# Kernel tuning notes

Hardware: AMD Instinct MI355X
Metric: run time of the kernel (lower is better)

The kernel has to match this reference:

```python
import jax, jax.numpy as jnp
import numpy as np

B, L, D_MODEL = 8, 256, 256
D_STATE, D_INNER, DT_RANK, D_CONV = 16, 512, 16, 4


def _ln(x, g, b, eps):
    mu = x.mean(-1, keepdims=True)
    var = ((x - mu) ** 2).mean(-1, keepdims=True)
    return (x - mu) * jax.lax.rsqrt(var + eps) * g + b


def _ssm(x, W_in, conv_w, conv_b, W_x, W_dt, b_dt, A_log, Dp, W_out):
    # x: (B, L, D_MODEL) -- standard Mamba selective-scan block
    xz = x @ W_in                                  # (B,L,2*Di)
    xc, z = jnp.split(xz, 2, axis=-1)
    K = conv_w.shape[-1]
    xp = jnp.pad(xc, ((0, 0), (K - 1, 0), (0, 0)))  # causal depthwise conv
    xc = sum(xp[:, k:k + L, :] * conv_w[:, k] for k in range(K)) + conv_b
    xc = jax.nn.silu(xc)
    x_dbl = xc @ W_x                               # (B,L,R+2S)
    dt, Bm, Cm = jnp.split(x_dbl, [DT_RANK, DT_RANK + D_STATE], axis=-1)
    dt = jax.nn.softplus(dt @ W_dt + b_dt)         # (B,L,Di)
    A = -jnp.exp(A_log)                            # (Di,S)
    dA = jnp.exp(dt[..., None] * A)                # (B,L,Di,S)
    dBx = dt[..., None] * Bm[:, :, None, :] * xc[..., None]

    def step(h, inp):
        dA_t, dBx_t, C_t = inp
        h = dA_t * h + dBx_t                       # (B,Di,S)
        y = jnp.einsum('bds,bs->bd', h, C_t)
        return h, y

    h0 = jnp.zeros((xc.shape[0], D_INNER, D_STATE), xc.dtype)
    xs = (dA.transpose(1, 0, 2, 3), dBx.transpose(1, 0, 2, 3), Cm.transpose(1, 0, 2))
    _, ys = jax.lax.scan(step, h0, xs)             # (L,B,Di)
    y = ys.transpose(1, 0, 2) + xc * Dp
    y = y * jax.nn.silu(z)
    return y @ W_out


def _basic(x, ln_g, ln_b, ssm_params):
    # Basic_Block: ReLU(SSM(LN(x))) + x  (drop_path=0, attn_drop=0)
    return jax.nn.relu(_ssm(_ln(x, ln_g, ln_b, 1e-6), *ssm_params)) + x


def setup_inputs() -> dict:
    key = jax.random.key(0)
    ks = jax.random.split(key, 32)

    def n(k, shape, s=0.02):
        return jax.random.normal(k, shape, dtype=jnp.float32) * s

    inp = {}
    inp['x_spa'] = jax.random.normal(ks[0], (B, L, D_MODEL), dtype=jnp.float32)
    inp['x_spe'] = jax.random.normal(ks[1], (B, L, D_MODEL), dtype=jnp.float32)
    i = 2
    A_init = jnp.log(jnp.tile(jnp.arange(1, D_STATE + 1, dtype=jnp.float32), (D_INNER, 1)))
    for p in ('spa', 'spe'):
        inp[p + '_ln_g'] = jnp.ones((D_MODEL,), jnp.float32)
        inp[p + '_ln_b'] = jnp.zeros((D_MODEL,), jnp.float32)
        inp[p + '_W_in'] = n(ks[i], (D_MODEL, 2 * D_INNER)); i += 1
        inp[p + '_conv_w'] = n(ks[i], (D_INNER, D_CONV), 0.1); i += 1
        inp[p + '_conv_b'] = jnp.zeros((D_INNER,), jnp.float32)
        inp[p + '_W_x'] = n(ks[i], (D_INNER, DT_RANK + 2 * D_STATE)); i += 1
        inp[p + '_W_dt'] = n(ks[i], (DT_RANK, D_INNER), 0.1); i += 1
        inp[p + '_b_dt'] = n(ks[i], (D_INNER,), 0.1); i += 1
        inp[p + '_A_log'] = A_init
        inp[p + '_D'] = jnp.ones((D_INNER,), jnp.float32)
        inp[p + '_W_out'] = n(ks[i], (D_INNER, D_MODEL)); i += 1
    inp['sc_W'] = n(ks[i], (D_MODEL, D_MODEL)); i += 1
    inp['sc_b'] = jnp.zeros((D_MODEL,), jnp.float32)
    inp['sc_ln_g'] = jnp.ones((D_MODEL,), jnp.float32)
    inp['sc_ln_b'] = jnp.zeros((D_MODEL,), jnp.float32)
    inp['fusion_W'] = n(ks[i], (D_MODEL, D_MODEL))
    return inp


def reference(x_spa, x_spe,
              spa_ln_g, spa_ln_b, spa_W_in, spa_conv_w, spa_conv_b, spa_W_x,
              spa_W_dt, spa_b_dt, spa_A_log, spa_D, spa_W_out,
              spe_ln_g, spe_ln_b, spe_W_in, spe_conv_w, spe_conv_b, spe_W_x,
              spe_W_dt, spe_b_dt, spe_A_log, spe_D, spe_W_out,
              sc_W, sc_b, sc_ln_g, sc_ln_b, fusion_W):
    # shared shortcut: Linear + LayerNorm (eps=1e-5)
    ident_spa = _ln(x_spa @ sc_W + sc_b, sc_ln_g, sc_ln_b, 1e-5)
    ident_spe = _ln(x_spe @ sc_W + sc_b, sc_ln_g, sc_ln_b, 1e-5)
    spa_p = (spa_W_in, spa_conv_w, spa_conv_b, spa_W_x, spa_W_dt, spa_b_dt, spa_A_log, spa_D, spa_W_out)
    spe_p = (spe_W_in, spe_conv_w, spe_conv_b, spe_W_x, spe_W_dt, spe_b_dt, spe_A_log, spe_D, spe_W_out)
    a = _basic(x_spa, spa_ln_g, spa_ln_b, spa_p)
    e = _basic(x_spe, spe_ln_g, spe_ln_b, spe_p)
    # fusion gate: mean-pool both branches, Linear(no bias) + sigmoid, broadcast-mul
    fw = jax.nn.sigmoid(((a.mean(1) + e.mean(1)) * 0.5) @ fusion_W)[:, None, :]
    a = a * fw
    e = e * fw
    return (a + ident_spa, e + ident_spe)
```

## Files before the change

kernel.cpp:

```cpp
#include <hip/hip_runtime.h>
#include <hip/hip_bf16.h>
#include <math.h>

#define BD 8
#define LD 256
#define DM 256
#define DS 16
#define DI 512
#define RK 16

#define NROWS (2*BD*LD)
#define HALF_ROWS (BD*LD)

typedef __attribute__((ext_vector_type(8))) short bhalf8;
typedef __attribute__((ext_vector_type(4))) float f32x4;

__device__ __forceinline__ float siluf(float x){ return x / (1.f + __expf(-x)); }
__device__ __forceinline__ float softplusf(float x){
  return fmaxf(x, 0.f) + log1pf(__expf(-fabsf(x)));
}
__device__ __forceinline__ unsigned short f2bf(float f){
  __hip_bfloat16 h = __float2bfloat16(f);
  return *reinterpret_cast<unsigned short*>(&h);
}


__global__ __launch_bounds__(256) void k_prep(
    const float* __restrict__ Wi_spa, const float* __restrict__ Wi_spe,
    const float* __restrict__ Wo_spa, const float* __restrict__ Wo_spe,
    const float* __restrict__ scW,
    const float* __restrict__ Wx_spa, const float* __restrict__ Wx_spe,
    const float* __restrict__ x_spa, const float* __restrict__ x_spe,
    const float* __restrict__ g_spa, const float* __restrict__ b_spa,
    const float* __restrict__ g_spe, const float* __restrict__ b_spe,
    unsigned short* __restrict__ Wt_i_spa, unsigned short* __restrict__ Wt_i_spe,
    unsigned short* __restrict__ Wt_o_spa, unsigned short* __restrict__ Wt_o_spe,
    unsigned short* __restrict__ scWt,
    unsigned short* __restrict__ Wxt_spa, unsigned short* __restrict__ Wxt_spe,
    unsigned short* __restrict__ xnbf, unsigned short* __restrict__ xbf,
    float* __restrict__ pooled)
{
  __shared__ __align__(16) unsigned char smem[59904];
  int b = blockIdx.x;
  int tid = threadIdx.x;
  if (b == 60){
    for (int i=tid; i<BD*DM; i+=256) pooled[i] = 0.f;
    return;
  }
  if (b >= 61){
    float (*xst)[260] = (float (*)[260])smem;
    float (*red)[16]  = (float (*)[16])(smem + 16640);
    float *mu = (float*)(smem + 17664);
    float *rs = (float*)(smem + 17728);
    int r0g = (b - 61) * 16;
    int branch = r0g >= HALF_ROWS;
    const float* xb = branch ? x_spe : x_spa;
    const float* g  = branch ? g_spe : g_spa;
    const float* be = branch ? b_spe : b_spa;
    int rr0 = branch ? r0g - HALF_ROWS : r0g;
    for (int p=0;p<4;p++){
      int i4 = tid + 256*p;
      int r = i4 >> 6, c4 = (i4 & 63)*4;
      *(float4*)&xst[r][c4] = *(const float4*)(xb + (rr0+r)*DM + c4);
    }
    __syncthreads();
    {
      int row = tid >> 4, seg = tid & 15;
      float s = 0.f, s2 = 0.f;
      #pragma unroll
      for (int i=0;i<4;i++){
        float4 v = *(float4*)&xst[row][seg*16 + i*4];
        s  += v.x+v.y+v.z+v.w;
        s2 += v.x*v.x + v.y*v.y + v.z*v.z + v.w*v.w;
      }
      red[row][seg] = s;
      __syncthreads();
      if (seg == 0){
        float t=0.f;
        #pragma unroll
        for (int i=0;i<16;i++) t += red[row][i];
        mu[row] = t * (1.f/DM);
      }
      __syncthreads();
      red[row][seg] = s2;
      __syncthreads();
      if (seg == 0){
        float t=0.f;
        #pragma unroll
        for (int i=0;i<16;i++) t += red[row][i];
        float m = mu[row];
        rs[row] = rsqrtf(t*(1.f/DM) - m*m + 1e-6f);
      }
    }
    __syncthreads();
    for (int p=0;p<4;p++){
      int i4 = tid + 256*p;
      int r = i4 >> 6, c4 = (i4 & 63)*4;
      float4 v  = *(float4*)&xst[r][c4];
      float4 gv = *(const float4*)(g + c4);
      float4 bv = *(const float4*)(be + c4);
      float m = mu[r], rv = rs[r];
      unsigned int rlo = (unsigned int)f2bf(v.x) | ((unsigned int)f2bf(v.y) << 16);
      unsigned int rhi = (unsigned int)f2bf(v.z) | ((unsigned int)f2bf(v.w) << 16);
      *(uint2*)&xbf[(r0g+r)*DM + c4] = make_uint2(rlo, rhi);
      unsigned int nlo = (unsigned int)f2bf((v.x-m)*rv*gv.x + bv.x)
                       | ((unsigned int)f2bf((v.y-m)*rv*gv.y + bv.y) << 16);
      unsigned int nhi = (unsigned int)f2bf((v.z-m)*rv*gv.z + bv.z)
                       | ((unsigned int)f2bf((v.w-m)*rv*gv.w + bv.w) << 16);
      *(uint2*)&xnbf[(r0g+r)*DM + c4] = make_uint2(nlo, nhi);
    }
    return;
  }
  if (b >= 52){
    int bb = b - 52;
    int branch = bb >> 2, chunk = bb & 3;
    int k0 = chunk*128;
    const float* Wx = branch ? Wx_spe : Wx_spa;
    unsigned short* Wxt = branch ? Wxt_spe : Wxt_spa;
    float (*tile2)[49] = (float (*)[49])(smem + 34816);
    for (int i=tid; i<128*48; i+=256){
      int kk = i/48, c = i - kk*48;
      tile2[kk][c] = Wx[(k0+kk)*48 + c];
    }
    __syncthreads();
    for (int i=tid; i<64*128; i+=256){
      int cc = i >> 7, kk = i & 127;
      float v = (cc < 48) ? tile2[kk][cc] : 0.f;
      int kg = k0 + kk;
      int ct = cc >> 4, m16 = cc & 15;
      int ks = kg >> 5, quad = (kg >> 3) & 3, j = kg & 7;
      Wxt[((ct*16 + ks)*64 + quad*16 + m16)*8 + j] = f2bf(v);
    }
    return;
  }
  unsigned short (*tile)[68] = (unsigned short (*)[68])smem;
  const float* W; unsigned short* Wt; int N, K, c0, k0;
  if (b < 32){
    int bb = b & 15;
    W  = (b < 16) ? Wi_spa  : Wi_spe;
    Wt = (b < 16) ? Wt_i_spa: Wt_i_spe;
    N = 1024; K = 256; c0 = (bb >> 2)*256; k0 = (bb & 3)*64;
  } else if (b < 48){
    int bb = b - 32; int h = bb >> 3; bb &= 7;
    W  = h ? Wo_spe  : Wo_spa;
    Wt = h ? Wt_o_spe: Wt_o_spa;
    N = 256; K = 512; c0 = 0; k0 = bb*64;
  } else {
    int bb = b - 48;
    W = scW; Wt = scWt;
    N = 256; K = 256; c0 = 0; k0 = bb*64;
  }
  int c = c0 + tid;
  #pragma unroll 8
  for (int kk=0; kk<64; kk++)
    tile[tid][kk] = f2bf(W[(k0+kk)*N + c]);
  __syncthreads();
  int ksegs = K >> 5;
  for (int p=0; p<16; p++){
    int i = tid + 256*p;
    int cl = i >> 4, kq = (i & 15)*4;
    int cg = c0 + cl;
    int ct = cg >> 4, m16 = cg & 15;
    int kg = k0 + kq;
    int ks = kg >> 5, quad = (kg >> 3) & 3, j = kg & 7;
    uint2 v = *(const uint2*)&tile[cl][kq];
    *(uint2*)&Wt[((ct*ksegs + ks)*64 + quad*16 + m16)*8 + j] = v;
  }
}

__global__ __launch_bounds__(256) void k_gemm1(
    const unsigned short* __restrict__ xnbf, const unsigned short* __restrict__ xbf,
    const unsigned short* __restrict__ Wt_spa, const unsigned short* __restrict__ Wt_spe,
    const unsigned short* __restrict__ scWt, const float* __restrict__ sc_b,
    const float* __restrict__ ln_g, const float* __restrict__ ln_b,
    float* __restrict__ xc_raw, float* __restrict__ szout, float* __restrict__ ident)
{
  __shared__ unsigned short At[16][264];
  __shared__ float Dt[16][260];
  __shared__ float red[16][16];
  __shared__ float mu[16], rs[16];
  int tid = threadIdx.x;
  int bi = blockIdx.x;
  int w = tid >> 6, lane = tid & 63;
  int m16 = lane & 15, quad = lane >> 4;
  if (bi < 1024){
    int rg = bi >> 2, cg = bi & 3;
    int r0 = rg * 16;
    int branch = (r0 >= HALF_ROWS);
    const unsigned short* Wt = branch ? Wt_spe : Wt_spa;
    for (int p=0;p<2;p++){
      int i = tid + 256*p;
      int r = i >> 5, oct = (i & 31)*8;
      *(uint4*)&At[r][oct] = *(const uint4*)&xnbf[(r0+r)*DM + oct];
    }
    __syncthreads();
    bhalf8 af[8];
    #pragma unroll
    for (int ks=0; ks<8; ks++)
      af[ks] = *(const bhalf8*)&At[m16][ks*32 + quad*8];
    f32x4 acc[4];
    #pragma unroll
    for (int ct=0; ct<4; ct++) acc[ct] = (f32x4)(0.f);
    #pragma unroll
    for (int ks=0; ks<8; ks++){
      #pragma unroll
      for (int ct=0; ct<4; ct++){
        int f = (cg*16 + w*4 + ct)*8 + ks;
        bhalf8 bf = *(const bhalf8*)&Wt[f*512 + lane*8];
        acc[ct] = __builtin_amdgcn_mfma_f32_16x16x32_bf16(af[ks], bf, acc[ct], 0,0,0);
      }
    }
    bool isz = (cg >= 2);
    float* outp = isz ? szout : xc_raw;
    int cbase = (cg & 1)*256 + w*64;
    #pragma unroll
    for (int ct=0; ct<4; ct++){
      #pragma unroll
      for (int e=0;e<4;e++){
        int row = r0 + quad*4 + e;
        int col = cbase + ct*16 + m16;
        float v = acc[ct][e];
        if (isz) v = siluf(v);
        outp[row*DI + col] = v;
      }
    }
  } else {
    int r0 = (bi - 1024) * 16;
    for (int p=0;p<2;p++){
      int i = tid + 256*p;
      int r = i >> 5, oct = (i & 31)*8;
      *(uint4*)&At[r][oct] = *(const uint4*)&xbf[(r0+r)*DM + oct];
    }
    __syncthreads();
    bhalf8 af[8];
    #pragma unroll
    for (int ks=0; ks<8; ks++)
      af[ks] = *(const bhalf8*)&At[m16][ks*32 + quad*8];
    f32x4 acc[4];
    #pragma unroll
    for (int ct=0; ct<4; ct++) acc[ct] = (f32x4)(0.f);
    #pragma unroll
    for (int ks=0; ks<8; ks++){
      #pragma unroll
      for (int ct=0; ct<4; ct++){
        int f = (w*4 + ct)*8 + ks;
        bhalf8 bf = *(const bhalf8*)&scWt[f*512 + lane*8];
        acc[ct] = __builtin_amdgcn_mfma_f32_16x16x32_bf16(af[ks], bf, acc[ct], 0,0,0);
      }
    }
    #pragma unroll
    for (int ct=0; ct<4; ct++){
      #pragma unroll
      for (int e=0;e<4;e++){
        int row = quad*4 + e;
        int col = w*64 + ct*16 + m16;
        Dt[row][col] = acc[ct][e] + sc_b[col];
      }
    }
    __syncthreads();
    {
      int row = tid >> 4, seg = tid & 15;
      float s = 0.f, s2 = 0.f;
      #pragma unroll
      for (int i=0;i<4;i++){
        float4 v = *(const float4*)&Dt[row][seg*16 + i*4];
        s  += v.x+v.y+v.z+v.w;
        s2 += v.x*v.x + v.y*v.y + v.z*v.z + v.w*v.w;
      }
      red[row][seg] = s;
      __syncthreads();
      if (seg == 0){
        float t=0.f;
        #pragma unroll
        for (int i=0;i<16;i++) t += red[row][i];
        mu[row] = t * (1.f/DM);
      }
      __syncthreads();
      red[row][seg] = s2;
      __syncthreads();
      if (seg == 0){
        float t=0.f;
        #pragma unroll
        for (int i=0;i<16;i++) t += red[row][i];
        float m = mu[row];
        rs[row] = rsqrtf(t*(1.f/DM) - m*m + 1e-5f);
      }
    }
    __syncthreads();
    float gg = ln_g[tid], bb = ln_b[tid];
    #pragma unroll
    for (int r=0;r<16;r++)
      ident[(r0+r)*DM + tid] = (Dt[r][tid]-mu[r])*rs[r]*gg + bb;
  }
}

__global__ __launch_bounds__(256) void k_convdbl(
    const float* __restrict__ cw_spa, const float* __restrict__ cb_spa,
    const float* __restrict__ cw_spe, const float* __restrict__ cb_spe,
    const float* __restrict__ xc_raw,
    const unsigned short* __restrict__ Wxt_spa, const unsigned short* __restrict__ Wxt_spe,
    const float* __restrict__ Wdt_spa, const float* __restrict__ bdt_spa,
    const float* __restrict__ Wdt_spe, const float* __restrict__ bdt_spe,
    float* __restrict__ xc, float* __restrict__ dt,
    float* __restrict__ Bm, float* __restrict__ Cm)
{
  __shared__ unsigned short At[16][520];
  __shared__ float xdbl[16][18];
  int tid = threadIdx.x;
  int r0 = blockIdx.x * 16;
  int branch = r0 >= HALF_ROWS;
  int l0 = r0 & (LD-1);
  const float* cw = branch ? cw_spe : cw_spa;
  const float* cb = branch ? cb_spe : cb_spa;
  const unsigned short* Wxt = branch ? Wxt_spe : Wxt_spa;
  const float* Wdt = branch ? Wdt_spe : Wdt_spa;
  const float* bdt = branch ? bdt_spe : bdt_spa;
  {
    int c = tid*2;
    float4 w0 = *(const float4*)(cw + 4*c);
    float4 w1 = *(const float4*)(cw + 4*(c+1));
    float2 bias = *(const float2*)(cb + c);
    float2 h0, h1, h2;
    if (l0 > 0){
      h0 = *(const float2*)(xc_raw + (r0-3)*DI + c);
      h1 = *(const float2*)(xc_raw + (r0-2)*DI + c);
      h2 = *(const float2*)(xc_raw + (r0-1)*DI + c);
    } else {
      h0 = make_float2(0.f,0.f); h1 = h0; h2 = h0;
    }
    #pragma unroll
    for (int r=0;r<16;r++){
      float2 cur = *(const float2*)(xc_raw + (r0+r)*DI + c);
      float vx = bias.x;
      vx = fmaf(h0.x, w0.x, vx); vx = fmaf(h1.x, w0.y, vx);
      vx = fmaf(h2.x, w0.z, vx); vx = fmaf(cur.x, w0.w, vx);
      float vy = bias.y;
      vy = fmaf(h0.y, w1.x, vy); vy = fmaf(h1.y, w1.y, vy);
      vy = fmaf(h2.y, w1.z, vy); vy = fmaf(cur.y, w1.w, vy);
      vx = siluf(vx); vy = siluf(vy);
      *(float2*)(xc + (r0+r)*DI + c) = make_float2(vx, vy);
      unsigned int pk = (unsigned int)f2bf(vx) | ((unsigned int)f2bf(vy) << 16);
      *(unsigned int*)&At[r][c] = pk;
      h0 = h1; h1 = h2; h2 = cur;
    }
  }
  __syncthreads();
  int w = tid >> 6, lane = tid & 63;
  int m16 = lane & 15, quad = lane >> 4;
  f32x4 acc = (f32x4)(0.f);
  #pragma unroll
  for (int ks=0; ks<16; ks++){
    bhalf8 a = *(const bhalf8*)&At[m16][ks*32 + quad*8];
    int f = w*16 + ks;
    bhalf8 bf = *(const bhalf8*)&Wxt[f*512 + lane*8];
    acc = __builtin_amdgcn_mfma_f32_16x16x32_bf16(a, bf, acc, 0,0,0);
  }
  #pragma unroll
  for (int e=0;e<4;e++){
    int row = quad*4 + e;
    float v = acc[e];
    if (w == 0)      xdbl[row][m16] = v;
    else if (w == 1) Bm[(r0+row)*DS + m16] = v;
    else if (w == 2) Cm[(r0+row)*DS + m16] = v;
  }
  __syncthreads();
  float wdt0[16], wdt1[16];
  #pragma unroll
  for (int j=0;j<16;j++){ wdt0[j]=Wdt[j*DI+tid]; wdt1[j]=Wdt[j*DI+tid+256]; }
  float b0 = bdt[tid], b1 = bdt[tid+256];
  #pragma unroll
  for (int r=0;r<16;r++){
    float a0=b0, a1=b1;
    #pragma unroll
    for (int j=0;j<16;j++){
      float xv = xdbl[r][j];
      a0 = fmaf(xv, wdt0[j], a0);
      a1 = fmaf(xv, wdt1[j], a1);
    }
    dt[(r0+r)*DI + tid]       = softplusf(a0);
    dt[(r0+r)*DI + tid + 256] = softplusf(a1);
  }
}

__global__ __launch_bounds__(256) void k_scan(
    const float* __restrict__ Alog_spa, const float* __restrict__ Dp_spa,
    const float* __restrict__ Alog_spe, const float* __restrict__ Dp_spe,
    const float* __restrict__ dt, const float* __restrict__ xc,
    const float* __restrict__ sz, const float* __restrict__ Bm,
    const float* __restrict__ Cm, unsigned short* __restrict__ ybf)
{
  __shared__ float ypbuf[2][16][257];
  __shared__ float Dsh[16];
  int tid = threadIdx.x;
  int bi = blockIdx.x;
  int branch = bi >> 8;
  int rem = bi & 255;
  int b = rem >> 5;
  int d0 = (rem & 31) * 16;
  const float* Alog = branch ? Alog_spe : Alog_spa;
  const float* Dp   = branch ? Dp_spe   : Dp_spa;
  int dg = tid >> 4, s = tid & 15;
  int d = d0 + dg;
  float A_ds = -__expf(Alog[d*DS + s]);
  if (tid < 16) Dsh[tid] = Dp[d0 + tid];
  int row0 = branch*HALF_ROWS + b*LD;
  int wcol = s*16 + ((dg + s) & 15);
  float h = 0.f;
  for (int c=0; c<16; c++){
    int rbase = row0 + c*16;
    int buf = c & 1;
    float rdt[16], rxc[16], rB[16], rC[16];
    #pragma unroll
    for (int li=0; li<16; li++){
      rdt[li] = dt[(rbase+li)*DI + d];
      rxc[li] = xc[(rbase+li)*DI + d];
      rB[li]  = Bm[(rbase+li)*DS + s];
      rC[li]  = Cm[(rbase+li)*DS + s];
    }
    float yp[16];
    #pragma unroll
    for (int li=0; li<16; li++){
      float dA = __expf(rdt[li] * A_ds);
      h = fmaf(dA, h, rdt[li] * rB[li] * rxc[li]);
      yp[li] = h * rC[li];
    }
    #pragma unroll
    for (int li=0; li<16; li++)
      ypbuf[buf][li][wcol] = yp[li];
    __syncthreads();
    float acc = 0.f;
    #pragma unroll
    for (int ss=0; ss<16; ss++)
      acc += ypbuf[buf][s][ss*16 + ((dg + ss) & 15)];
    float xcv = rxc[s];
    float szv = sz[(rbase+s)*DI + d0 + dg];
    float yv = fmaf(xcv, Dsh[dg], acc) * szv;
    ybf[(rbase+s)*DI + d0 + dg] = f2bf(yv);
  }
}

__global__ __launch_bounds__(256) void k_wout(
    const unsigned short* __restrict__ Wt_spa, const unsigned short* __restrict__ Wt_spe,
    const float* __restrict__ x_spa, const float* __restrict__ x_spe,
    const unsigned short* __restrict__ ybf, float* __restrict__ ae,
    float* __restrict__ pooled)
{
  __shared__ unsigned short At[16][520];
  int tid = threadIdx.x;
  int bi = blockIdx.x;
  int r0 = (bi >> 1) * 16;
  int ch = bi & 1;
  int branch = (r0 >= HALF_ROWS);
  const unsigned short* Wt = branch ? Wt_spe : Wt_spa;
  const float* xb = branch ? x_spe : x_spa;
  int rr0 = branch ? r0 - HALF_ROWS : r0;
  for (int p=0;p<4;p++){
    int i = tid + 256*p;
    int r = i >> 6, oct = (i & 63)*8;
    *(uint4*)&At[r][oct] = *(const uint4*)&ybf[(r0+r)*DI + oct];
  }
  __syncthreads();
  int w = tid >> 6, lane = tid & 63;
  int m16 = lane & 15, quad = lane >> 4;
  bhalf8 af[16];
  #pragma unroll
  for (int ks=0; ks<16; ks++)
    af[ks] = *(const bhalf8*)&At[m16][ks*32 + quad*8];
  f32x4 acc[2];
  #pragma unroll
  for (int ct=0; ct<2; ct++) acc[ct] = (f32x4)(0.f);
  #pragma unroll
  for (int ks=0; ks<16; ks++){
    #pragma unroll
    for (int ct=0; ct<2; ct++){
      int f = (ch*8 + w*2 + ct)*16 + ks;
      bhalf8 bf = *(const bhalf8*)&Wt[f*512 + lane*8];
      acc[ct] = __builtin_amdgcn_mfma_f32_16x16x32_bf16(af[ks], bf, acc[ct], 0,0,0);
    }
  }
  float ps0 = 0.f, ps1 = 0.f;
  #pragma unroll
  for (int ct=0; ct<2; ct++){
    #pragma unroll
    for (int e=0;e<4;e++){
      int row = quad*4 + e;
      int col = ch*128 + w*32 + ct*16 + m16;
      float v = fmaxf(acc[ct][e], 0.f) + xb[(rr0+row)*DM + col];
      ae[(r0+row)*DM + col] = v;
      if (ct == 0) ps0 += v; else ps1 += v;
    }
  }
  ps0 += __shfl_xor(ps0, 16, 64); ps0 += __shfl_xor(ps0, 32, 64);
  ps1 += __shfl_xor(ps1, 16, 64); ps1 += __shfl_xor(ps1, 32, 64);
  if (quad == 0){
    int bidx = (r0 >> 8) & 7;
    atomicAdd(&pooled[bidx*DM + ch*128 + w*32 + m16],      ps0);
    atomicAdd(&pooled[bidx*DM + ch*128 + w*32 + 16 + m16], ps1);
  }
}

__global__ __launch_bounds__(256) void k_gate(const float* __restrict__ pooled,
    const float* __restrict__ fW, float* __restrict__ fw)
{
  __shared__ float p[DM];
  int b=blockIdx.x, c=threadIdx.x;
  p[c] = pooled[b*DM+c] * (0.5f/LD);
  __syncthreads();
  float a=0.f;
  for(int k=0;k<DM;k+=4){
    a = fmaf(p[k+0], fW[(k+0)*DM+c], a);
    a = fmaf(p[k+1], fW[(k+1)*DM+c], a);
    a = fmaf(p[k+2], fW[(k+2)*DM+c], a);
    a = fmaf(p[k+3], fW[(k+3)*DM+c], a);
  }
  fw[b*DM+c]=1.f/(1.f+__expf(-a));
}

__global__ __launch_bounds__(256) void k_final(const float* __restrict__ ae,
    const float* __restrict__ ident, const float* __restrict__ fw, float* __restrict__ out)
{
  int idx4 = blockIdx.x*256 + threadIdx.x;
  int row = idx4 >> 6;
  int b = (row >> 8) & 7;
  int c4 = (idx4 & 63) * 4;
  float4 av = *(const float4*)(ae + idx4*4);
  float4 iv = *(const float4*)(ident + idx4*4);
  float4 fv = *(const float4*)(fw + b*DM + c4);
  float4 o;
  o.x = fmaf(av.x, fv.x, iv.x);
  o.y = fmaf(av.y, fv.y, iv.y);
  o.z = fmaf(av.z, fv.z, iv.z);
  o.w = fmaf(av.w, fv.w, iv.w);
  *(float4*)(out + idx4*4) = o;
}

extern "C" void kernel_launch(void* const* d_in, const int* in_sizes, int n_in,
                              void* d_out, int out_size, void* d_ws, size_t ws_size,
                              hipStream_t stream) {
  const float* x_spa     = (const float*)d_in[0];
  const float* x_spe     = (const float*)d_in[1];
  const float* spa_ln_g  = (const float*)d_in[2];
  const float* spa_ln_b  = (const float*)d_in[3];
  const float* spa_W_in  = (const float*)d_in[4];
  const float* spa_cw    = (const float*)d_in[5];
  const float* spa_cb    = (const float*)d_in[6];
  const float* spa_W_x   = (const float*)d_in[7];
  const float* spa_W_dt  = (const float*)d_in[8];
  const float* spa_b_dt  = (const float*)d_in[9];
  const float* spa_A_log = (const float*)d_in[10];
  const float* spa_D     = (const float*)d_in[11];
  const float* spa_W_out = (const float*)d_in[12];
  const float* spe_ln_g  = (const float*)d_in[13];
  const float* spe_ln_b  = (const float*)d_in[14];
  const float* spe_W_in  = (const float*)d_in[15];
  const float* spe_cw    = (const float*)d_in[16];
  const float* spe_cb    = (const float*)d_in[17];
  const float* spe_W_x   = (const float*)d_in[18];
  const float* spe_W_dt  = (const float*)d_in[19];
  const float* spe_b_dt  = (const float*)d_in[20];
  const float* spe_A_log = (const float*)d_in[21];
  const float* spe_D     = (const float*)d_in[22];
  const float* spe_W_out = (const float*)d_in[23];
  const float* sc_W      = (const float*)d_in[24];
  const float* sc_b      = (const float*)d_in[25];
  const float* sc_ln_g   = (const float*)d_in[26];
  const float* sc_ln_b   = (const float*)d_in[27];
  const float* fusion_W  = (const float*)d_in[28];

  float* ws = (float*)d_ws;
  float* ident  = ws;
  float* xc_raw = ident  + NROWS*DM;
  float* sz     = xc_raw + NROWS*DI;
  float* xc     = sz     + NROWS*DI;
  float* dt     = xc     + NROWS*DI;
  float* Bm     = dt     + NROWS*DI;
  float* Cm     = Bm     + NROWS*DS;
  float* pooled = Cm     + NROWS*DS;
  float* fw     = pooled + BD*DM;
  unsigned short* Wt_i_spa = (unsigned short*)(fw + BD*DM);
  unsigned short* Wt_i_spe = Wt_i_spa + 1024*256;
  unsigned short* Wt_o_spa = Wt_i_spe + 1024*256;
  unsigned short* Wt_o_spe = Wt_o_spa + 256*512;
  unsigned short* scWt     = Wt_o_spe + 256*512;
  unsigned short* Wxt_spa  = scWt     + 256*256;
  unsigned short* Wxt_spe  = Wxt_spa  + 64*512;
  unsigned short* xnbf     = Wxt_spe  + 64*512;
  unsigned short* xbf      = xnbf     + NROWS*DM;

  float* out = (float*)d_out;

  k_prep<<<317, 256, 0, stream>>>(spa_W_in, spe_W_in, spa_W_out, spe_W_out, sc_W,
                                  spa_W_x, spe_W_x, x_spa, x_spe,
                                  spa_ln_g, spa_ln_b, spe_ln_g, spe_ln_b,
                                  Wt_i_spa, Wt_i_spe, Wt_o_spa, Wt_o_spe, scWt,
                                  Wxt_spa, Wxt_spe, xnbf, xbf, pooled);
  k_gemm1<<<1280, 256, 0, stream>>>(xnbf, xbf, Wt_i_spa, Wt_i_spe, scWt, sc_b,
                                    sc_ln_g, sc_ln_b, xc_raw, sz, ident);
  k_convdbl<<<NROWS/16, 256, 0, stream>>>(spa_cw, spa_cb, spe_cw, spe_cb, xc_raw,
                                          Wxt_spa, Wxt_spe,
                                          spa_W_dt, spa_b_dt, spe_W_dt, spe_b_dt,
                                          xc, dt, Bm, Cm);
  unsigned short* ybf = (unsigned short*)xc_raw;
  k_scan<<<512, 256, 0, stream>>>(spa_A_log, spa_D, spe_A_log, spe_D, dt, xc, sz, Bm, Cm, ybf);
  float* ae = dt;
  k_wout<<<512, 256, 0, stream>>>(Wt_o_spa, Wt_o_spe, x_spa, x_spe, ybf, ae, pooled);
  k_gate<<<BD, 256, 0, stream>>>(pooled, fusion_W, fw);
  k_final<<<NROWS*DM/1024, 256, 0, stream>>>(ae, ident, fw, out);
}
```

Before: 197.1 us.

## Store scan inputs time-major per channel and fuse gate into final kernel

The intermediate buffers (xc_raw, sz, xc, dt, B, C) are now stored as [batch][channel][L] instead of [row][channel]. The scan kernel can then read 16 consecutive timesteps per thread with float4 loads instead of strided scalar loads, and the producer kernels write float4 runs along L. The gate computation is also fused into the final elementwise kernel, which removes one launch, but each of the 128 blocks now recomputes the 256x256 gate matvec. The transposed writes in gemm1 and convdbl are less coalesced across a wavefront, which may cost write bandwidth.

```diff
diff --git a/kernel.cpp b/kernel.cpp
--- a/kernel.cpp
+++ b/kernel.cpp
@@ -173,7 +173,7 @@
     const unsigned short* __restrict__ Wt_spa, const unsigned short* __restrict__ Wt_spe,
     const unsigned short* __restrict__ scWt, const float* __restrict__ sc_b,
     const float* __restrict__ ln_g, const float* __restrict__ ln_b,
-    float* __restrict__ xc_raw, float* __restrict__ szout, float* __restrict__ ident)
+    float* __restrict__ xcrT, float* __restrict__ szT, float* __restrict__ ident)
 {
   __shared__ unsigned short At[16][264];
   __shared__ float Dt[16][260];
@@ -211,18 +211,20 @@
       }
     }
     bool isz = (cg >= 2);
-    float* outp = isz ? szout : xc_raw;
+    float* outp = isz ? szT : xcrT;
     int cbase = (cg & 1)*256 + w*64;
+    int bb = r0 >> 8, l0 = r0 & (LD-1);
     #pragma unroll
     for (int ct=0; ct<4; ct++){
-      #pragma unroll
-      for (int e=0;e<4;e++){
-        int row = r0 + quad*4 + e;
-        int col = cbase + ct*16 + m16;
-        float v = acc[ct][e];
-        if (isz) v = siluf(v);
-        outp[row*DI + col] = v;
-      }
+      int col = cbase + ct*16 + m16;
+      float4 v;
+      if (isz){
+        v.x = siluf(acc[ct][0]); v.y = siluf(acc[ct][1]);
+        v.z = siluf(acc[ct][2]); v.w = siluf(acc[ct][3]);
+      } else {
+        v.x = acc[ct][0]; v.y = acc[ct][1]; v.z = acc[ct][2]; v.w = acc[ct][3];
+      }
+      *(float4*)&outp[(bb*DI + col)*LD + l0 + quad*4] = v;
     }
   } else {
     int r0 = (bi - 1024) * 16;
@@ -287,28 +289,29 @@
       }
     }
     __syncthreads();
-    float gg = ln_g[tid], bb = ln_b[tid];
+    float gg = ln_g[tid], bb2 = ln_b[tid];
     #pragma unroll
     for (int r=0;r<16;r++)
-      ident[(r0+r)*DM + tid] = (Dt[r][tid]-mu[r])*rs[r]*gg + bb;
+      ident[(r0+r)*DM + tid] = (Dt[r][tid]-mu[r])*rs[r]*gg + bb2;
   }
 }
 
 __global__ __launch_bounds__(256) void k_convdbl(
     const float* __restrict__ cw_spa, const float* __restrict__ cb_spa,
     const float* __restrict__ cw_spe, const float* __restrict__ cb_spe,
-    const float* __restrict__ xc_raw,
+    const float* __restrict__ xcrT,
     const unsigned short* __restrict__ Wxt_spa, const unsigned short* __restrict__ Wxt_spe,
     const float* __restrict__ Wdt_spa, const float* __restrict__ bdt_spa,
     const float* __restrict__ Wdt_spe, const float* __restrict__ bdt_spe,
-    float* __restrict__ xc, float* __restrict__ dt,
-    float* __restrict__ Bm, float* __restrict__ Cm)
+    float* __restrict__ xcT, float* __restrict__ dtT,
+    float* __restrict__ BmT, float* __restrict__ CmT)
 {
   __shared__ unsigned short At[16][520];
   __shared__ float xdbl[16][18];
   int tid = threadIdx.x;
   int r0 = blockIdx.x * 16;
   int branch = r0 >= HALF_ROWS;
+  int bb = r0 >> 8;
   int l0 = r0 & (LD-1);
   const float* cw = branch ? cw_spe : cw_spa;
   const float* cb = branch ? cb_spe : cb_spa;
@@ -316,32 +319,45 @@
   const float* Wdt = branch ? Wdt_spe : Wdt_spa;
   const float* bdt = branch ? bdt_spe : bdt_spa;
   {
-    int c = tid*2;
-    float4 w0 = *(const float4*)(cw + 4*c);
-    float4 w1 = *(const float4*)(cw + 4*(c+1));
-    float2 bias = *(const float2*)(cb + c);
-    float2 h0, h1, h2;
-    if (l0 > 0){
-      h0 = *(const float2*)(xc_raw + (r0-3)*DI + c);
-      h1 = *(const float2*)(xc_raw + (r0-2)*DI + c);
-      h2 = *(const float2*)(xc_raw + (r0-1)*DI + c);
-    } else {
-      h0 = make_float2(0.f,0.f); h1 = h0; h2 = h0;
+    int c0 = tid*2;
+    float v0[16], v1[16];
+    #pragma unroll
+    for (int cc=0; cc<2; cc++){
+      int c = c0 + cc;
+      const float* src = xcrT + (bb*DI + c)*LD;
+      float4 cwv = *(const float4*)(cw + 4*c);
+      float bias = cb[c];
+      float x[19];
+      if (l0 > 0){
+        x[0] = src[l0-3]; x[1] = src[l0-2]; x[2] = src[l0-1];
+      } else { x[0]=0.f; x[1]=0.f; x[2]=0.f; }
+      #pragma unroll
+      for (int q=0;q<4;q++){
+        float4 v = *(const float4*)(src + l0 + q*4);
+        x[3+q*4+0]=v.x; x[3+q*4+1]=v.y; x[3+q*4+2]=v.z; x[3+q*4+3]=v.w;
+      }
+      float* dst = cc ? v1 : v0;
+      #pragma unroll
+      for (int r=0;r<16;r++){
+        float a = bias;
+        a = fmaf(x[r+0], cwv.x, a);
+        a = fmaf(x[r+1], cwv.y, a);
+        a = fmaf(x[r+2], cwv.z, a);
+        a = fmaf(x[r+3], cwv.w, a);
+        dst[r] = siluf(a);
+      }
+    }
+    float* d0p = xcT + (bb*DI + c0)*LD + l0;
+    float* d1p = xcT + (bb*DI + c0+1)*LD + l0;
+    #pragma unroll
+    for (int q=0;q<4;q++){
+      *(float4*)(d0p + q*4) = make_float4(v0[q*4],v0[q*4+1],v0[q*4+2],v0[q*4+3]);
+      *(float4*)(d1p + q*4) = make_float4(v1[q*4],v1[q*4+1],v1[q*4+2],v1[q*4+3]);
     }
     #pragma unroll
     for (int r=0;r<16;r++){
-      float2 cur = *(const float2*)(xc_raw + (r0+r)*DI + c);
-      float vx = bias.x;
-      vx = fmaf(h0.x, w0.x, vx); vx = fmaf(h1.x, w0.y, vx);
-      vx = fmaf(h2.x, w0.z, vx); vx = fmaf(cur.x, w0.w, vx);
-      float vy = bias.y;
-      vy = fmaf(h0.y, w1.x, vy); vy = fmaf(h1.y, w1.y, vy);
-      vy = fmaf(h2.y, w1.z, vy); vy = fmaf(cur.y, w1.w, vy);
-      vx = siluf(vx); vy = siluf(vy);
-      *(float2*)(xc + (r0+r)*DI + c) = make_float2(vx, vy);
-      unsigned int pk = (unsigned int)f2bf(vx) | ((unsigned int)f2bf(vy) << 16);
-      *(unsigned int*)&At[r][c] = pk;
-      h0 = h1; h1 = h2; h2 = cur;
+      unsigned int pk = (unsigned int)f2bf(v0[r]) | ((unsigned int)f2bf(v1[r]) << 16);
+      *(unsigned int*)&At[r][c0] = pk;
     }
   }
   __syncthreads();
@@ -355,19 +371,20 @@
     bhalf8 bf = *(const bhalf8*)&Wxt[f*512 + lane*8];
     acc = __builtin_amdgcn_mfma_f32_16x16x32_bf16(a, bf, acc, 0,0,0);
   }
-  #pragma unroll
-  for (int e=0;e<4;e++){
-    int row = quad*4 + e;
-    float v = acc[e];
-    if (w == 0)      xdbl[row][m16] = v;
-    else if (w == 1) Bm[(r0+row)*DS + m16] = v;
-    else if (w == 2) Cm[(r0+row)*DS + m16] = v;
+  if (w == 0){
+    #pragma unroll
+    for (int e=0;e<4;e++) xdbl[quad*4 + e][m16] = acc[e];
+  } else if (w == 1){
+    *(float4*)&BmT[(bb*DS + m16)*LD + l0 + quad*4] = make_float4(acc[0],acc[1],acc[2],acc[3]);
+  } else if (w == 2){
+    *(float4*)&CmT[(bb*DS + m16)*LD + l0 + quad*4] = make_float4(acc[0],acc[1],acc[2],acc[3]);
   }
   __syncthreads();
   float wdt0[16], wdt1[16];
   #pragma unroll
   for (int j=0;j<16;j++){ wdt0[j]=Wdt[j*DI+tid]; wdt1[j]=Wdt[j*DI+tid+256]; }
   float b0 = bdt[tid], b1 = bdt[tid+256];
+  float dv0[16], dv1[16];
   #pragma unroll
   for (int r=0;r<16;r++){
     float a0=b0, a1=b1;
@@ -377,17 +394,24 @@
       a0 = fmaf(xv, wdt0[j], a0);
       a1 = fmaf(xv, wdt1[j], a1);
     }
-    dt[(r0+r)*DI + tid]       = softplusf(a0);
-    dt[(r0+r)*DI + tid + 256] = softplusf(a1);
+    dv0[r] = softplusf(a0);
+    dv1[r] = softplusf(a1);
+  }
+  float* t0 = dtT + (bb*DI + tid)*LD + l0;
+  float* t1 = dtT + (bb*DI + tid + 256)*LD + l0;
+  #pragma unroll
+  for (int q=0;q<4;q++){
+    *(float4*)(t0 + q*4) = make_float4(dv0[q*4],dv0[q*4+1],dv0[q*4+2],dv0[q*4+3]);
+    *(float4*)(t1 + q*4) = make_float4(dv1[q*4],dv1[q*4+1],dv1[q*4+2],dv1[q*4+3]);
   }
 }
 
 __global__ __launch_bounds__(256) void k_scan(
     const float* __restrict__ Alog_spa, const float* __restrict__ Dp_spa,
     const float* __restrict__ Alog_spe, const float* __restrict__ Dp_spe,
-    const float* __restrict__ dt, const float* __restrict__ xc,
-    const float* __restrict__ sz, const float* __restrict__ Bm,
-    const float* __restrict__ Cm, unsigned short* __restrict__ ybf)
+    const float* __restrict__ dtT, const float* __restrict__ xcT,
+    const float* __restrict__ szT, const float* __restrict__ BmT,
+    const float* __restrict__ CmT, unsigned short* __restrict__ ybf)
 {
   __shared__ float ypbuf[2][16][257];
   __shared__ float Dsh[16];
@@ -403,19 +427,25 @@
   int d = d0 + dg;
   float A_ds = -__expf(Alog[d*DS + s]);
   if (tid < 16) Dsh[tid] = Dp[d0 + tid];
+  int bb = branch*BD + b;
   int row0 = branch*HALF_ROWS + b*LD;
+  const float* dtp = dtT + (bb*DI + d)*LD;
+  const float* xcp = xcT + (bb*DI + d)*LD;
+  const float* szp = szT + (bb*DI + d)*LD;
+  const float* Bp  = BmT + (bb*DS + s)*LD;
+  const float* Cp  = CmT + (bb*DS + s)*LD;
   int wcol = s*16 + ((dg + s) & 15);
   float h = 0.f;
   for (int c=0; c<16; c++){
-    int rbase = row0 + c*16;
+    int l0c = c*16;
     int buf = c & 1;
     float rdt[16], rxc[16], rB[16], rC[16];
     #pragma unroll
-    for (int li=0; li<16; li++){
-      rdt[li] = dt[(rbase+li)*DI + d];
-      rxc[li] = xc[(rbase+li)*DI + d];
-      rB[li]  = Bm[(rbase+li)*DS + s];
-      rC[li]  = Cm[(rbase+li)*DS + s];
+    for (int q=0;q<4;q++){
+      *(float4*)&rdt[q*4] = *(const float4*)(dtp + l0c + q*4);
+      *(float4*)&rxc[q*4] = *(const float4*)(xcp + l0c + q*4);
+      *(float4*)&rB[q*4]  = *(const float4*)(Bp  + l0c + q*4);
+      *(float4*)&rC[q*4]  = *(const float4*)(Cp  + l0c + q*4);
     }
     float yp[16];
     #pragma unroll
@@ -433,9 +463,9 @@
     for (int ss=0; ss<16; ss++)
       acc += ypbuf[buf][s][ss*16 + ((dg + ss) & 15)];
     float xcv = rxc[s];
-    float szv = sz[(rbase+s)*DI + d0 + dg];
+    float szv = szp[l0c + s];
     float yv = fmaf(xcv, Dsh[dg], acc) * szv;
-    ybf[(rbase+s)*DI + d0 + dg] = f2bf(yv);
+    ybf[(row0 + l0c + s)*DI + d0 + dg] = f2bf(yv);
   }
 }
 
@@ -499,39 +529,40 @@
   }
 }
 
-__global__ __launch_bounds__(256) void k_gate(const float* __restrict__ pooled,
-    const float* __restrict__ fW, float* __restrict__ fw)
+__global__ __launch_bounds__(256) void k_gatefinal(const float* __restrict__ pooled,
+    const float* __restrict__ fW, const float* __restrict__ ae,
+    const float* __restrict__ ident, float* __restrict__ out)
 {
   __shared__ float p[DM];
-  int b=blockIdx.x, c=threadIdx.x;
+  __shared__ float fwsh[DM];
+  int bi = blockIdx.x, c = threadIdx.x;
+  int r0 = bi * 32;
+  int b = (r0 >> 8) & 7;
   p[c] = pooled[b*DM+c] * (0.5f/LD);
   __syncthreads();
-  float a=0.f;
-  for(int k=0;k<DM;k+=4){
+  float a = 0.f;
+  for (int k=0;k<DM;k+=4){
     a = fmaf(p[k+0], fW[(k+0)*DM+c], a);
     a = fmaf(p[k+1], fW[(k+1)*DM+c], a);
     a = fmaf(p[k+2], fW[(k+2)*DM+c], a);
     a = fmaf(p[k+3], fW[(k+3)*DM+c], a);
   }
-  fw[b*DM+c]=1.f/(1.f+__expf(-a));
-}
-
-__global__ __launch_bounds__(256) void k_final(const float* __restrict__ ae,
-    const float* __restrict__ ident, const float* __restrict__ fw, float* __restrict__ out)
-{
-  int idx4 = blockIdx.x*256 + threadIdx.x;
-  int row = idx4 >> 6;
-  int b = (row >> 8) & 7;
-  int c4 = (idx4 & 63) * 4;
-  float4 av = *(const float4*)(ae + idx4*4);
-  float4 iv = *(const float4*)(ident + idx4*4);
-  float4 fv = *(const float4*)(fw + b*DM + c4);
-  float4 o;
-  o.x = fmaf(av.x, fv.x, iv.x);
-  o.y = fmaf(av.y, fv.y, iv.y);
-  o.z = fmaf(av.z, fv.z, iv.z);
-  o.w = fmaf(av.w, fv.w, iv.w);
-  *(float4*)(out + idx4*4) = o;
+  fwsh[c] = 1.f/(1.f+__expf(-a));
+  __syncthreads();
+  for (int q=0;q<8;q++){
+    int i4 = c + 256*q;
+    int r = i4 >> 6, c4 = (i4 & 63)*4;
+    int base = (r0 + r)*DM + c4;
+    float4 av = *(const float4*)(ae + base);
+    float4 iv = *(const float4*)(ident + base);
+    float4 fv = *(const float4*)&fwsh[c4];
+    float4 o;
+    o.x = fmaf(av.x, fv.x, iv.x);
+    o.y = fmaf(av.y, fv.y, iv.y);
+    o.z = fmaf(av.z, fv.z, iv.z);
+    o.w = fmaf(av.w, fv.w, iv.w);
+    *(float4*)(out + base) = o;
+  }
 }
 
 extern "C" void kernel_launch(void* const* d_in, const int* in_sizes, int n_in,
@@ -569,13 +600,13 @@
 
   float* ws = (float*)d_ws;
   float* ident  = ws;
-  float* xc_raw = ident  + NROWS*DM;
-  float* sz     = xc_raw + NROWS*DI;
-  float* xc     = sz     + NROWS*DI;
-  float* dt     = xc     + NROWS*DI;
-  float* Bm     = dt     + NROWS*DI;
-  float* Cm     = Bm     + NROWS*DS;
-  float* pooled = Cm     + NROWS*DS;
+  float* xcrT   = ident  + NROWS*DM;
+  float* szT    = xcrT   + NROWS*DI;
+  float* xcT    = szT    + NROWS*DI;
+  float* dtT    = xcT    + NROWS*DI;
+  float* BmT    = dtT    + NROWS*DI;
+  float* CmT    = BmT    + NROWS*DS;
+  float* pooled = CmT    + NROWS*DS;
   float* fw     = pooled + BD*DM;
   unsigned short* Wt_i_spa = (unsigned short*)(fw + BD*DM);
   unsigned short* Wt_i_spe = Wt_i_spa + 1024*256;
@@ -595,15 +626,15 @@
                                   Wt_i_spa, Wt_i_spe, Wt_o_spa, Wt_o_spe, scWt,
                                   Wxt_spa, Wxt_spe, xnbf, xbf, pooled);
   k_gemm1<<<1280, 256, 0, stream>>>(xnbf, xbf, Wt_i_spa, Wt_i_spe, scWt, sc_b,
-                                    sc_ln_g, sc_ln_b, xc_raw, sz, ident);
-  k_convdbl<<<NROWS/16, 256, 0, stream>>>(spa_cw, spa_cb, spe_cw, spe_cb, xc_raw,
+                                    sc_ln_g, sc_ln_b, xcrT, szT, ident);
+  k_convdbl<<<NROWS/16, 256, 0, stream>>>(spa_cw, spa_cb, spe_cw, spe_cb, xcrT,
                                           Wxt_spa, Wxt_spe,
                                           spa_W_dt, spa_b_dt, spe_W_dt, spe_b_dt,
-                                          xc, dt, Bm, Cm);
-  unsigned short* ybf = (unsigned short*)xc_raw;
-  k_scan<<<512, 256, 0, stream>>>(spa_A_log, spa_D, spe_A_log, spe_D, dt, xc, sz, Bm, Cm, ybf);
-  float* ae = dt;
+                                          xcT, dtT, BmT, CmT);
+  unsigned short* ybf = (unsigned short*)xcrT;
+  k_scan<<<512, 256, 0, stream>>>(spa_A_log, spa_D, spe_A_log, spe_D,
+                                  dtT, xcT, szT, BmT, CmT, ybf);
+  float* ae = dtT;
   k_wout<<<512, 256, 0, stream>>>(Wt_o_spa, Wt_o_spe, x_spa, x_spe, ybf, ae, pooled);
-  k_gate<<<BD, 256, 0, stream>>>(pooled, fusion_W, fw);
-  k_final<<<NROWS*DM/1024, 256, 0, stream>>>(ae, ident, fw, out);
-}
+  k_gatefinal<<<128, 256, 0, stream>>>(pooled, fusion_W, ae, ident, out);
+}
```

Result: slower. 229.5 us (+16.4%).

## Double-buffer scan input loads and fuse gate computation into final kernel

Applied to the files above, without the earlier changes.

The scan kernel now prefetches the next chunk's dt, xc, B, C and gate values into a second register buffer while computing the current chunk, so global load latency overlaps the recurrence. The separate gate and final kernels are merged into one: each of 128 blocks recomputes the sigmoid gate for its batch in shared memory, then applies it to 32 rows. This removes one launch and the fw round-trip, at the cost of redundant gate matvecs and higher register pressure in the scan.

```diff
diff --git a/kernel.cpp b/kernel.cpp
--- a/kernel.cpp
+++ b/kernel.cpp
@@ -287,10 +287,10 @@
       }
     }
     __syncthreads();
-    float gg = ln_g[tid], bb = ln_b[tid];
+    float gg = ln_g[tid], bb2 = ln_b[tid];
     #pragma unroll
     for (int r=0;r<16;r++)
-      ident[(r0+r)*DM + tid] = (Dt[r][tid]-mu[r])*rs[r]*gg + bb;
+      ident[(r0+r)*DM + tid] = (Dt[r][tid]-mu[r])*rs[r]*gg + bb2;
   }
 }
 
@@ -406,23 +406,36 @@
   int row0 = branch*HALF_ROWS + b*LD;
   int wcol = s*16 + ((dg + s) & 15);
   float h = 0.f;
+  float rdt[2][16], rxc[2][16], rB[2][16], rC[2][16], rsz[2];
+  #pragma unroll
+  for (int li=0; li<16; li++){
+    rdt[0][li] = dt[(row0+li)*DI + d];
+    rxc[0][li] = xc[(row0+li)*DI + d];
+    rB[0][li]  = Bm[(row0+li)*DS + s];
+    rC[0][li]  = Cm[(row0+li)*DS + s];
+  }
+  rsz[0] = sz[(row0+s)*DI + d0 + dg];
+  #pragma unroll
   for (int c=0; c<16; c++){
+    int buf = c & 1, nb = buf ^ 1;
     int rbase = row0 + c*16;
-    int buf = c & 1;
-    float rdt[16], rxc[16], rB[16], rC[16];
+    float yp[16];
     #pragma unroll
     for (int li=0; li<16; li++){
-      rdt[li] = dt[(rbase+li)*DI + d];
-      rxc[li] = xc[(rbase+li)*DI + d];
-      rB[li]  = Bm[(rbase+li)*DS + s];
-      rC[li]  = Cm[(rbase+li)*DS + s];
-    }
-    float yp[16];
-    #pragma unroll
-    for (int li=0; li<16; li++){
-      float dA = __expf(rdt[li] * A_ds);
-      h = fmaf(dA, h, rdt[li] * rB[li] * rxc[li]);
-      yp[li] = h * rC[li];
+      float dA = __expf(rdt[buf][li] * A_ds);
+      h = fmaf(dA, h, rdt[buf][li] * rB[buf][li] * rxc[buf][li]);
+      yp[li] = h * rC[buf][li];
+    }
+    if (c < 15){
+      int nbase = rbase + 16;
+      #pragma unroll
+      for (int li=0; li<16; li++){
+        rdt[nb][li] = dt[(nbase+li)*DI + d];
+        rxc[nb][li] = xc[(nbase+li)*DI + d];
+        rB[nb][li]  = Bm[(nbase+li)*DS + s];
+        rC[nb][li]  = Cm[(nbase+li)*DS + s];
+      }
+      rsz[nb] = sz[(nbase+s)*DI + d0 + dg];
     }
     #pragma unroll
     for (int li=0; li<16; li++)
@@ -432,9 +445,7 @@
     #pragma unroll
     for (int ss=0; ss<16; ss++)
       acc += ypbuf[buf][s][ss*16 + ((dg + ss) & 15)];
-    float xcv = rxc[s];
-    float szv = sz[(rbase+s)*DI + d0 + dg];
-    float yv = fmaf(xcv, Dsh[dg], acc) * szv;
+    float yv = fmaf(rxc[buf][s], Dsh[dg], acc) * rsz[buf];
     ybf[(rbase+s)*DI + d0 + dg] = f2bf(yv);
   }
 }
@@ -499,39 +510,40 @@
   }
 }
 
-__global__ __launch_bounds__(256) void k_gate(const float* __restrict__ pooled,
-    const float* __restrict__ fW, float* __restrict__ fw)
+__global__ __launch_bounds__(256) void k_gatefinal(const float* __restrict__ pooled,
+    const float* __restrict__ fW, const float* __restrict__ ae,
+    const float* __restrict__ ident, float* __restrict__ out)
 {
   __shared__ float p[DM];
-  int b=blockIdx.x, c=threadIdx.x;
+  __shared__ float fwsh[DM];
+  int bi = blockIdx.x, c = threadIdx.x;
+  int r0 = bi * 32;
+  int b = (r0 >> 8) & 7;
   p[c] = pooled[b*DM+c] * (0.5f/LD);
   __syncthreads();
-  float a=0.f;
-  for(int k=0;k<DM;k+=4){
+  float a = 0.f;
+  for (int k=0;k<DM;k+=4){
     a = fmaf(p[k+0], fW[(k+0)*DM+c], a);
     a = fmaf(p[k+1], fW[(k+1)*DM+c], a);
     a = fmaf(p[k+2], fW[(k+2)*DM+c], a);
     a = fmaf(p[k+3], fW[(k+3)*DM+c], a);
   }
-  fw[b*DM+c]=1.f/(1.f+__expf(-a));
-}
-
-__global__ __launch_bounds__(256) void k_final(const float* __restrict__ ae,
-    const float* __restrict__ ident, const float* __restrict__ fw, float* __restrict__ out)
-{
-  int idx4 = blockIdx.x*256 + threadIdx.x;
-  int row = idx4 >> 6;
-  int b = (row >> 8) & 7;
-  int c4 = (idx4 & 63) * 4;
-  float4 av = *(const float4*)(ae + idx4*4);
-  float4 iv = *(const float4*)(ident + idx4*4);
-  float4 fv = *(const float4*)(fw + b*DM + c4);
-  float4 o;
-  o.x = fmaf(av.x, fv.x, iv.x);
-  o.y = fmaf(av.y, fv.y, iv.y);
-  o.z = fmaf(av.z, fv.z, iv.z);
-  o.w = fmaf(av.w, fv.w, iv.w);
-  *(float4*)(out + idx4*4) = o;
+  fwsh[c] = 1.f/(1.f+__expf(-a));
+  __syncthreads();
+  for (int q=0;q<8;q++){
+    int i4 = c + 256*q;
+    int r = i4 >> 6, c4 = (i4 & 63)*4;
+    int base = (r0 + r)*DM + c4;
+    float4 av = *(const float4*)(ae + base);
+    float4 iv = *(const float4*)(ident + base);
+    float4 fv = *(const float4*)&fwsh[c4];
+    float4 o;
+    o.x = fmaf(av.x, fv.x, iv.x);
+    o.y = fmaf(av.y, fv.y, iv.y);
+    o.z = fmaf(av.z, fv.z, iv.z);
+    o.w = fmaf(av.w, fv.w, iv.w);
+    *(float4*)(out + base) = o;
+  }
 }
 
 extern "C" void kernel_launch(void* const* d_in, const int* in_sizes, int n_in,
@@ -604,6 +616,5 @@
   k_scan<<<512, 256, 0, stream>>>(spa_A_log, spa_D, spe_A_log, spe_D, dt, xc, sz, Bm, Cm, ybf);
   float* ae = dt;
   k_wout<<<512, 256, 0, stream>>>(Wt_o_spa, Wt_o_spe, x_spa, x_spe, ybf, ae, pooled);
-  k_gate<<<BD, 256, 0, stream>>>(pooled, fusion_W, fw);
-  k_final<<<NROWS*DM/1024, 256, 0, stream>>>(ae, ident, fw, out);
-}
+  k_gatefinal<<<128, 256, 0, stream>>>(pooled, fusion_W, ae, ident, out);
+}
```

Result: no change. 198.0 us, median of 3 (+0.5%).
